# Kernel tuning notes

Hardware: AMD Instinct MI355X
Metric: run time of the kernel (lower is better)

## Reference

```python
import jax, jax.numpy as jnp
import numpy as np

DIM = 1024
HIDDEN = 2816
NUM_EXPERTS = 8
TOP_K = 2
BATCH, SEQ = 2, 2048


def setup_inputs() -> dict:
    key = jax.random.key(0)
    kx, k1, k2, k3, kg = jax.random.split(key, 5)
    x = jax.random.normal(kx, (BATCH, SEQ, DIM), dtype=jnp.float32)
    # merged expert weights, layout (num_experts * hidden, dim) as in torch module
    w1 = jax.random.normal(k1, (NUM_EXPERTS * HIDDEN, DIM), dtype=jnp.float32) * 0.02
    w2 = jax.random.normal(k2, (NUM_EXPERTS * HIDDEN, DIM), dtype=jnp.float32) * 0.02
    w3 = jax.random.normal(k3, (NUM_EXPERTS * HIDDEN, DIM), dtype=jnp.float32) * 0.02
    gate_w = jax.random.normal(kg, (NUM_EXPERTS, DIM), dtype=jnp.float32) * 0.02
    return {"x": x, "w1": w1, "w2": w2, "w3": w3, "gate_w": gate_w}


def reference(x, w1, w2, w3, gate_w):
    input_shape = x.shape
    xt = x.reshape(-1, input_shape[-1])  # (T, D)
    T = xt.shape[0]
    # gating: softmax in fp32, top-k, renormalize selected weights
    logits = xt @ gate_w.T  # (T, E)
    probs = jax.nn.softmax(logits.astype(jnp.float32), axis=-1)
    weights, selected = jax.lax.top_k(probs, TOP_K)  # (T, K)
    weights = weights / jnp.sum(weights, axis=-1, keepdims=True)
    weights = weights.astype(x.dtype)
    # combine weights per expert: (T, E)
    combine = jnp.sum(jax.nn.one_hot(selected, NUM_EXPERTS, dtype=x.dtype) * weights[..., None], axis=1)
    # per-expert SwiGLU FFN: h = silu(x W1_e^T) * (x W3_e^T); out_e = h @ W2_e
    W1 = w1.reshape(NUM_EXPERTS, HIDDEN, DIM)
    W2 = w2.reshape(NUM_EXPERTS, HIDDEN, DIM)
    W3 = w3.reshape(NUM_EXPERTS, HIDDEN, DIM)
    y = jnp.zeros((T, DIM), dtype=x.dtype)
    for e in range(NUM_EXPERTS):  # fixed small expert loop
        h = jax.nn.silu(xt @ W1[e].T) * (xt @ W3[e].T)  # (T, H)
        y = y + (h @ W2[e]) * combine[:, e:e + 1]
    return y.reshape(input_shape)
```

## Files before the change

kernel.cpp:

```cpp
#include <hip/hip_runtime.h>
#include <cstddef>
#include <cstdint>

#define T_TOK 4096
#define DIM   1024
#define HID   2816
#define NE    8
#define TOPK  2
#define CAP   9216
#define NRT   72
#define BM    128
#define BN    64
#define BK    32

#define WS_COUNTS  0
#define WS_CURSORS 64
#define WS_OFFSETS 128
#define WS_TILE_E  256
#define WS_SEL     1024
#define WS_WTS     33792
#define WS_ATOK    66560
#define WS_AW      103424
#define WS_XHI     140288
#define WS_XLO     8528896
#define WS_IMG     16917504

typedef __attribute__((ext_vector_type(8))) short bf16x8;
typedef __attribute__((ext_vector_type(8))) unsigned short u16x8;
typedef __attribute__((ext_vector_type(4))) float f32x4;

#define GL16(gp, lp) __builtin_amdgcn_global_load_lds( \
    (const __attribute__((address_space(1))) unsigned int*)(gp), \
    (__attribute__((address_space(3))) unsigned int*)(lp), 16, 0, 0)

__device__ __forceinline__ unsigned short f2bf(float f) {
  unsigned int u = __builtin_bit_cast(unsigned int, f);
  unsigned int r = u + 0x7FFFu + ((u >> 16) & 1u);
  return (unsigned short)(r >> 16);
}
__device__ __forceinline__ float bf2f(unsigned short s) {
  unsigned int u = ((unsigned int)s) << 16;
  return __builtin_bit_cast(float, u);
}
__device__ __forceinline__ void split2(float f, unsigned short& hi, unsigned short& lo) {
  hi = f2bf(f);
  lo = f2bf(f - bf2f(hi));
}

__global__ __launch_bounds__(256) void gate_kernel(
    const float* __restrict__ x, const float* __restrict__ gw,
    int* __restrict__ sel, float* __restrict__ wts, int* __restrict__ counts)
{
  const int wave = threadIdx.x >> 6;
  const int lane = threadIdx.x & 63;
  const int t = blockIdx.x * 4 + wave;
  const float* xr = x + (size_t)t * DIM;
  float acc[NE] = {0.f, 0.f, 0.f, 0.f, 0.f, 0.f, 0.f, 0.f};
#pragma unroll 4
  for (int j = 0; j < DIM / 64; ++j) {
    const int d = lane + 64 * j;
    const float xv = xr[d];
#pragma unroll
    for (int e = 0; e < NE; ++e) acc[e] = fmaf(xv, gw[e * DIM + d], acc[e]);
  }
#pragma unroll
  for (int m = 32; m > 0; m >>= 1) {
#pragma unroll
    for (int e = 0; e < NE; ++e) acc[e] += __shfl_xor(acc[e], m, 64);
  }
  if (lane == 0) {
    float mx = acc[0];
#pragma unroll
    for (int e = 1; e < NE; ++e) mx = fmaxf(mx, acc[e]);
    float ex[NE];
#pragma unroll
    for (int e = 0; e < NE; ++e) ex[e] = __expf(acc[e] - mx);
    int e0 = 0; float p0 = ex[0];
#pragma unroll
    for (int e = 1; e < NE; ++e) if (ex[e] > p0) { p0 = ex[e]; e0 = e; }
    int e1 = -1; float p1 = -1.f;
#pragma unroll
    for (int e = 0; e < NE; ++e) if (e != e0 && ex[e] > p1) { p1 = ex[e]; e1 = e; }
    const float inv = 1.f / (p0 + p1);
    sel[2 * t + 0] = e0; sel[2 * t + 1] = e1;
    wts[2 * t + 0] = p0 * inv; wts[2 * t + 1] = p1 * inv;
    atomicAdd(&counts[e0], 1);
    atomicAdd(&counts[e1], 1);
  }
}

__global__ void offsets_kernel(const int* __restrict__ counts,
                               int* __restrict__ offsets, int* __restrict__ cursors,
                               int* __restrict__ tile_e)
{
  if (threadIdx.x == 0 && blockIdx.x == 0) {
    int off = 0;
    for (int e = 0; e < NE; ++e) {
      offsets[e] = off;
      cursors[e] = off;
      off += (counts[e] + 127) & ~127;
    }
    offsets[NE] = off;
    for (int t = 0; t < NRT; ++t) {
      const int r = t * BM;
      int ee = 0;
      while (ee < NE - 1 && r >= offsets[ee + 1]) ++ee;
      tile_e[t] = ee;
    }
  }
}

__global__ __launch_bounds__(256) void scatter_kernel(
    const int* __restrict__ sel, const float* __restrict__ wts,
    int* __restrict__ cursors, int* __restrict__ atok, float* __restrict__ aw)
{
  const int t = blockIdx.x * 256 + threadIdx.x;
  if (t < T_TOK) {
#pragma unroll
    for (int k = 0; k < TOPK; ++k) {
      const int e = sel[2 * t + k];
      const int pos = atomicAdd(&cursors[e], 1);
      atok[pos] = t;
      aw[pos] = wts[2 * t + k];
    }
  }
}

__global__ __launch_bounds__(256) void convert_x_kernel(
    const float* __restrict__ x, unsigned short* __restrict__ xhi,
    unsigned short* __restrict__ xlo)
{
  const size_t t = (size_t)blockIdx.x * 256 + threadIdx.x;
  const float* s = x + t * 8;
  u16x8 hi, lo;
#pragma unroll
  for (int q = 0; q < 8; ++q) {
    unsigned short h, l;
    split2(s[q], h, l);
    hi[q] = h; lo[q] = l;
  }
  *(u16x8*)&xhi[t * 8] = hi;
  *(u16x8*)&xlo[t * 8] = lo;
}

__global__ __launch_bounds__(256) void convert_w13_kernel(
    const float* __restrict__ w, unsigned short* __restrict__ img,
    int hc0, int nct1)
{
  const int g = blockIdx.x * 256 + threadIdx.x;
  const int c = g & 255;
  const int t = g >> 8;
  const int n15 = c & 15, ks = (c >> 4) & 3, nb = c >> 6;
  const int kt = t & 31;
  const int ec = t >> 5;
  const int ct = ec % nct1, e = ec / nct1;
  const float* src = w + ((size_t)e * HID + hc0 + ct * 64 + nb * 16 + n15) * DIM + kt * 32 + ks * 8;
  u16x8 hi, lo;
#pragma unroll
  for (int q = 0; q < 8; ++q) {
    unsigned short h, l;
    split2(src[q], h, l);
    hi[q] = h; lo[q] = l;
  }
  *(u16x8*)&img[(size_t)t * 4096 + c * 8] = hi;
  *(u16x8*)&img[(size_t)t * 4096 + 2048 + c * 8] = lo;
}

__global__ __launch_bounds__(256) void convert_w2_kernel(
    const float* __restrict__ w2, unsigned short* __restrict__ img,
    int hc0, int nkt2)
{
  const int f = blockIdx.x * 256 + threadIdx.x;
  const int n15 = f & 15;
  int t = f >> 4;
  const int ks = t & 3; t >>= 2;
  const int nb = t & 3; t >>= 2;
  const int kt = t % nkt2; t /= nkt2;
  const int ct2 = t & 15;
  const int e = t >> 4;
  const float* src = w2 + ((size_t)e * HID + hc0 + kt * 32 + ks * 8) * DIM + ct2 * 64 + nb * 16 + n15;
  u16x8 hi, lo;
#pragma unroll
  for (int q = 0; q < 8; ++q) {
    unsigned short h, l;
    split2(src[(size_t)q * DIM], h, l);
    hi[q] = h; lo[q] = l;
  }
  const size_t tile = ((size_t)(e * 16 + ct2) * nkt2 + kt) * 4096;
  const int off = nb * 512 + ks * 128 + n15 * 8;
  *(u16x8*)&img[tile + off] = hi;
  *(u16x8*)&img[tile + 2048 + off] = lo;
}

__global__ __launch_bounds__(256) void gemm1_kernel(
    const unsigned short* __restrict__ xhi, const unsigned short* __restrict__ xlo,
    const unsigned short* __restrict__ w1img, const unsigned short* __restrict__ w3img,
    const int* __restrict__ atok, const int* __restrict__ tile_e,
    const int* __restrict__ offsets, unsigned short* __restrict__ himg, int nct1)
{
  __shared__ __align__(16) unsigned short sAh[4096], sAl[4096];
  __shared__ __align__(16) unsigned short sB1h[2048], sB1l[2048], sB3h[2048], sB3l[2048];
  __shared__ int sToks[BM];

  const int orig = blockIdx.x;
  const int wg = (orig & 7) * (gridDim.x >> 3) + (orig >> 3);
  const int ct = wg / NRT, rt = wg % NRT;
  if (rt * BM >= offsets[NE]) return;
  const int nkt2 = nct1 * 2;
  const int tid = threadIdx.x, lane = tid & 63;
  const int wv = tid >> 6, wr = wv >> 1, wc = wv & 1;
  const int e = tile_e[rt];

  if (tid < BM) {
    const int tk = atok[rt * BM + tid];
    sToks[tid] = tk < 0 ? 0 : tk;
  }
  __syncthreads();

  const int rb0 = wv * 2;
  size_t asrc[2];
#pragma unroll
  for (int i = 0; i < 2; ++i) {
    const int row = (rb0 + i) * 16 + (lane & 15);
    asrc[i] = (size_t)sToks[row] * DIM + ((lane >> 4) * 8);
  }
  const size_t btile0 = ((size_t)(e * nct1 + ct) * 32) * 4096;
  const size_t boff = btile0 + wv * 512 + (size_t)lane * 8;

  const f32x4 vz = {0.f, 0.f, 0.f, 0.f};
  f32x4 acc1[4][2], acc3[4][2];
#pragma unroll
  for (int i = 0; i < 4; ++i)
#pragma unroll
    for (int j = 0; j < 2; ++j) { acc1[i][j] = vz; acc3[i][j] = vz; }

  for (int kt = 0; kt < DIM / BK; ++kt) {
    __syncthreads();
#pragma unroll
    for (int i = 0; i < 2; ++i) {
      GL16(xhi + asrc[i] + kt * 32, &sAh[(rb0 + i) * 512]);
      GL16(xlo + asrc[i] + kt * 32, &sAl[(rb0 + i) * 512]);
    }
    const size_t bk = boff + (size_t)kt * 4096;
    GL16(w1img + bk,        &sB1h[wv * 512]);
    GL16(w1img + bk + 2048, &sB1l[wv * 512]);
    GL16(w3img + bk,        &sB3h[wv * 512]);
    GL16(w3img + bk + 2048, &sB3l[wv * 512]);
    __syncthreads();

    bf16x8 ah[4], al[4], g1h[2], g1l[2], g3h[2], g3l[2];
#pragma unroll
    for (int ar = 0; ar < 4; ++ar) {
      const int rb = wr * 4 + ar;
      ah[ar] = *(const bf16x8*)&sAh[rb * 512 + lane * 8];
      al[ar] = *(const bf16x8*)&sAl[rb * 512 + lane * 8];
    }
#pragma unroll
    for (int bc = 0; bc < 2; ++bc) {
      const int cb = wc * 2 + bc;
      g1h[bc] = *(const bf16x8*)&sB1h[cb * 512 + lane * 8];
      g1l[bc] = *(const bf16x8*)&sB1l[cb * 512 + lane * 8];
      g3h[bc] = *(const bf16x8*)&sB3h[cb * 512 + lane * 8];
      g3l[bc] = *(const bf16x8*)&sB3l[cb * 512 + lane * 8];
    }
#pragma unroll
    for (int ar = 0; ar < 4; ++ar)
#pragma unroll
      for (int bc = 0; bc < 2; ++bc) {
        acc1[ar][bc] = __builtin_amdgcn_mfma_f32_16x16x32_bf16(ah[ar], g1h[bc], acc1[ar][bc], 0, 0, 0);
        acc1[ar][bc] = __builtin_amdgcn_mfma_f32_16x16x32_bf16(ah[ar], g1l[bc], acc1[ar][bc], 0, 0, 0);
        acc1[ar][bc] = __builtin_amdgcn_mfma_f32_16x16x32_bf16(al[ar], g1h[bc], acc1[ar][bc], 0, 0, 0);
        acc3[ar][bc] = __builtin_amdgcn_mfma_f32_16x16x32_bf16(ah[ar], g3h[bc], acc3[ar][bc], 0, 0, 0);
        acc3[ar][bc] = __builtin_amdgcn_mfma_f32_16x16x32_bf16(ah[ar], g3l[bc], acc3[ar][bc], 0, 0, 0);
        acc3[ar][bc] = __builtin_amdgcn_mfma_f32_16x16x32_bf16(al[ar], g3h[bc], acc3[ar][bc], 0, 0, 0);
      }
  }

  const size_t hbase = ((size_t)rt * nkt2 + (ct * 2 + wc)) * 8192;
#pragma unroll
  for (int ar = 0; ar < 4; ++ar)
#pragma unroll
    for (int bc = 0; bc < 2; ++bc)
#pragma unroll
      for (int r = 0; r < 4; ++r) {
        const float g = acc1[ar][bc][r];
        const float u = acc3[ar][bc][r];
        const float s = g / (1.f + __expf(-g));
        unsigned short h_, l_;
        split2(s * u, h_, l_);
        const int idx = (wr * 4 + ar) * 512 + (bc * 2 + ((lane >> 3) & 1)) * 128
                      + ((lane >> 4) * 4 + r) * 8 + (lane & 7);
        himg[hbase + idx] = h_;
        himg[hbase + 4096 + idx] = l_;
      }
}

__global__ __launch_bounds__(256) void gemm2_kernel(
    const unsigned short* __restrict__ himg, const unsigned short* __restrict__ w2img,
    const int* __restrict__ atok, const float* __restrict__ aw,
    const int* __restrict__ tile_e, const int* __restrict__ offsets,
    float* __restrict__ y, int nkt2)
{
  __shared__ __align__(16) unsigned short sAh[4096], sAl[4096];
  __shared__ __align__(16) unsigned short sBh[2048], sBl[2048];

  const int orig = blockIdx.x;
  const int wg = (orig & 7) * (gridDim.x >> 3) + (orig >> 3);
  const int ct2 = wg / NRT, rt = wg % NRT;
  if (rt * BM >= offsets[NE]) return;
  const int tid = threadIdx.x, lane = tid & 63;
  const int wv = tid >> 6, wr = wv >> 1, wc = wv & 1;
  const int e = tile_e[rt];

  const int rb0 = wv * 2;
  const size_t atile0 = (size_t)rt * nkt2 * 8192;
  const size_t btile0 = ((size_t)(e * 16 + ct2) * nkt2) * 4096;
  const size_t lane8 = (size_t)lane * 8;

  const f32x4 vz = {0.f, 0.f, 0.f, 0.f};
  f32x4 acc[4][2];
#pragma unroll
  for (int i = 0; i < 4; ++i)
#pragma unroll
    for (int j = 0; j < 2; ++j) acc[i][j] = vz;

  for (int kt = 0; kt < nkt2; ++kt) {
    __syncthreads();
    const size_t ab = atile0 + (size_t)kt * 8192;
#pragma unroll
    for (int i = 0; i < 2; ++i) {
      GL16(himg + ab + (rb0 + i) * 512 + lane8,        &sAh[(rb0 + i) * 512]);
      GL16(himg + ab + 4096 + (rb0 + i) * 512 + lane8, &sAl[(rb0 + i) * 512]);
    }
    const size_t bb = btile0 + (size_t)kt * 4096 + wv * 512 + lane8;
    GL16(w2img + bb,        &sBh[wv * 512]);
    GL16(w2img + bb + 2048, &sBl[wv * 512]);
    __syncthreads();

    bf16x8 ah[4], al[4], bh_[2], bl_[2];
#pragma unroll
    for (int ar = 0; ar < 4; ++ar) {
      const int rb = wr * 4 + ar;
      ah[ar] = *(const bf16x8*)&sAh[rb * 512 + lane * 8];
      al[ar] = *(const bf16x8*)&sAl[rb * 512 + lane * 8];
    }
#pragma unroll
    for (int bc = 0; bc < 2; ++bc) {
      const int cb = wc * 2 + bc;
      bh_[bc] = *(const bf16x8*)&sBh[cb * 512 + lane * 8];
      bl_[bc] = *(const bf16x8*)&sBl[cb * 512 + lane * 8];
    }
#pragma unroll
    for (int ar = 0; ar < 4; ++ar)
#pragma unroll
      for (int bc = 0; bc < 2; ++bc) {
        acc[ar][bc] = __builtin_amdgcn_mfma_f32_16x16x32_bf16(ah[ar], bh_[bc], acc[ar][bc], 0, 0, 0);
        acc[ar][bc] = __builtin_amdgcn_mfma_f32_16x16x32_bf16(ah[ar], bl_[bc], acc[ar][bc], 0, 0, 0);
        acc[ar][bc] = __builtin_amdgcn_mfma_f32_16x16x32_bf16(al[ar], bh_[bc], acc[ar][bc], 0, 0, 0);
      }
  }

#pragma unroll
  for (int ar = 0; ar < 4; ++ar)
#pragma unroll
    for (int r = 0; r < 4; ++r) {
      const int grow = rt * BM + wr * 64 + ar * 16 + (lane >> 4) * 4 + r;
      const int tok = atok[grow];
      if (tok >= 0) {
        const float wgt = aw[grow];
#pragma unroll
        for (int bc = 0; bc < 2; ++bc) {
          const int col = ct2 * BN + wc * 32 + bc * 16 + (lane & 15);
          atomicAdd(y + (size_t)tok * DIM + col, acc[ar][bc][r] * wgt);
        }
      }
    }
}

extern "C" void kernel_launch(void* const* d_in, const int* in_sizes, int n_in,
                              void* d_out, int out_size, void* d_ws, size_t ws_size,
                              hipStream_t stream) {
  const float* x  = (const float*)d_in[0];
  const float* w1 = (const float*)d_in[1];
  const float* w2 = (const float*)d_in[2];
  const float* w3 = (const float*)d_in[3];
  const float* gw = (const float*)d_in[4];
  float* y = (float*)d_out;

  char* ws = (char*)d_ws;
  int*   counts  = (int*)(ws + WS_COUNTS);
  int*   cursors = (int*)(ws + WS_CURSORS);
  int*   offsets = (int*)(ws + WS_OFFSETS);
  int*   tile_e  = (int*)(ws + WS_TILE_E);
  int*   sel     = (int*)(ws + WS_SEL);
  float* wts     = (float*)(ws + WS_WTS);
  int*   atok    = (int*)(ws + WS_ATOK);
  float* aw      = (float*)(ws + WS_AW);
  unsigned short* xhi = (unsigned short*)(ws + WS_XHI);
  unsigned short* xlo = (unsigned short*)(ws + WS_XLO);

  static const int chs[6] = {2816, 1408, 704, 256, 128, 64};
  int CH = 64;
  for (int i = 0; i < 6; ++i) {
    const size_t need = (size_t)WS_IMG + (size_t)chs[i] * 135168ull;
    if (need <= ws_size) { CH = chs[i]; break; }
  }
  const int nct1 = CH / 64, nkt2 = CH / 32;
  const size_t wimg_b = (size_t)CH * 32768ull;
  unsigned short* w1img = (unsigned short*)(ws + WS_IMG);
  unsigned short* w3img = (unsigned short*)(ws + WS_IMG + wimg_b);
  unsigned short* w2img = (unsigned short*)(ws + WS_IMG + 2 * wimg_b);
  unsigned short* himg  = (unsigned short*)(ws + WS_IMG + 3 * wimg_b);

  hipMemsetAsync(counts, 0, 8 * sizeof(int), stream);
  hipMemsetAsync(atok, 0xFF, CAP * sizeof(int), stream);
  hipMemsetAsync(y, 0, (size_t)T_TOK * DIM * sizeof(float), stream);

  gate_kernel<<<T_TOK / 4, 256, 0, stream>>>(x, gw, sel, wts, counts);
  offsets_kernel<<<1, 64, 0, stream>>>(counts, offsets, cursors, tile_e);
  scatter_kernel<<<T_TOK / 256, 256, 0, stream>>>(sel, wts, cursors, atok, aw);
  convert_x_kernel<<<(T_TOK * DIM / 8) / 256, 256, 0, stream>>>(x, xhi, xlo);

  for (int hc0 = 0; hc0 < HID; hc0 += CH) {
    const int wblk = 8 * nct1 * 32;
    convert_w13_kernel<<<wblk, 256, 0, stream>>>(w1, w1img, hc0, nct1);
    convert_w13_kernel<<<wblk, 256, 0, stream>>>(w3, w3img, hc0, nct1);
    convert_w2_kernel<<<128 * nkt2, 256, 0, stream>>>(w2, w2img, hc0, nkt2);
    gemm1_kernel<<<NRT * nct1, 256, 0, stream>>>(xhi, xlo, w1img, w3img, atok, tile_e, offsets, himg, nct1);
    gemm2_kernel<<<NRT * 16, 256, 0, stream>>>(himg, w2img, atok, aw, tile_e, offsets, y, nkt2);
  }
}
```

Baseline: 1.111 ms.

## Store weight hi/lo splits in plain row-major layout with coalesced conversion

Weight conversion now writes separate hi and lo bf16 planes in simple row-major layout: W1/W3 are converted with fully contiguous reads and writes, and W2 is transposed through an LDS tile so both the reads and the writes are coalesced. Before this, the conversion kernels wrote tiled images, and the W2 path read with a DIM stride. The GEMM kernels now load B fragments from these row-major planes using strided row addresses instead of contiguous tile blocks. The aim is to make the fp32-to-bf16 conversion passes cheaper, at the risk of less contiguous B loads inside the GEMMs.

```diff
diff --git a/kernel.cpp b/kernel.cpp
--- a/kernel.cpp
+++ b/kernel.cpp
@@ -143,58 +143,67 @@
   *(u16x8*)&xlo[t * 8] = lo;
 }
 
-__global__ __launch_bounds__(256) void convert_w13_kernel(
-    const float* __restrict__ w, unsigned short* __restrict__ img,
-    int hc0, int nct1)
-{
-  const int g = blockIdx.x * 256 + threadIdx.x;
-  const int c = g & 255;
-  const int t = g >> 8;
-  const int n15 = c & 15, ks = (c >> 4) & 3, nb = c >> 6;
-  const int kt = t & 31;
-  const int ec = t >> 5;
-  const int ct = ec % nct1, e = ec / nct1;
-  const float* src = w + ((size_t)e * HID + hc0 + ct * 64 + nb * 16 + n15) * DIM + kt * 32 + ks * 8;
+__global__ __launch_bounds__(256) void convert_w13s_kernel(
+    const float* __restrict__ w, unsigned short* __restrict__ hi_img,
+    unsigned short* __restrict__ lo_img, int hc0, int CH)
+{
+  const int e = blockIdx.y;
+  const size_t off = ((size_t)blockIdx.x * 256 + threadIdx.x) * 8;
+  const float* s = w + ((size_t)e * HID + hc0) * DIM + off;
   u16x8 hi, lo;
 #pragma unroll
   for (int q = 0; q < 8; ++q) {
     unsigned short h, l;
-    split2(src[q], h, l);
+    split2(s[q], h, l);
     hi[q] = h; lo[q] = l;
   }
-  *(u16x8*)&img[(size_t)t * 4096 + c * 8] = hi;
-  *(u16x8*)&img[(size_t)t * 4096 + 2048 + c * 8] = lo;
-}
-
-__global__ __launch_bounds__(256) void convert_w2_kernel(
-    const float* __restrict__ w2, unsigned short* __restrict__ img,
-    int hc0, int nkt2)
-{
-  const int f = blockIdx.x * 256 + threadIdx.x;
-  const int n15 = f & 15;
-  int t = f >> 4;
-  const int ks = t & 3; t >>= 2;
-  const int nb = t & 3; t >>= 2;
-  const int kt = t % nkt2; t /= nkt2;
-  const int ct2 = t & 15;
-  const int e = t >> 4;
-  const float* src = w2 + ((size_t)e * HID + hc0 + kt * 32 + ks * 8) * DIM + ct2 * 64 + nb * 16 + n15;
-  u16x8 hi, lo;
-#pragma unroll
-  for (int q = 0; q < 8; ++q) {
-    unsigned short h, l;
-    split2(src[(size_t)q * DIM], h, l);
-    hi[q] = h; lo[q] = l;
-  }
-  const size_t tile = ((size_t)(e * 16 + ct2) * nkt2 + kt) * 4096;
-  const int off = nb * 512 + ks * 128 + n15 * 8;
-  *(u16x8*)&img[tile + off] = hi;
-  *(u16x8*)&img[tile + 2048 + off] = lo;
+  const size_t d = (size_t)e * CH * DIM + off;
+  *(u16x8*)&hi_img[d] = hi;
+  *(u16x8*)&lo_img[d] = lo;
+}
+
+__global__ __launch_bounds__(256) void convert_w2t_kernel(
+    const float* __restrict__ w2, unsigned short* __restrict__ hi_img,
+    unsigned short* __restrict__ lo_img, int hc0, int CH)
+{
+  __shared__ float tile[64][65];
+  const int kb = blockIdx.x;
+  const int nb = blockIdx.y;
+  const int e  = blockIdx.z;
+  const int tid = threadIdx.x;
+
+  const int r0 = tid >> 4;
+  const int c4 = (tid & 15) * 4;
+#pragma unroll
+  for (int i = 0; i < 4; ++i) {
+    const int k = r0 + i * 16;
+    const float4 v = *(const float4*)(w2 + ((size_t)e * HID + hc0 + kb * 64 + k) * DIM + nb * 64 + c4);
+    tile[k][c4 + 0] = v.x; tile[k][c4 + 1] = v.y;
+    tile[k][c4 + 2] = v.z; tile[k][c4 + 3] = v.w;
+  }
+  __syncthreads();
+
+#pragma unroll
+  for (int i = 0; i < 2; ++i) {
+    const int c = tid + 256 * i;
+    const int n = c >> 3, k8 = (c & 7) * 8;
+    u16x8 hi, lo;
+#pragma unroll
+    for (int q = 0; q < 8; ++q) {
+      unsigned short h, l;
+      split2(tile[k8 + q][n], h, l);
+      hi[q] = h; lo[q] = l;
+    }
+    const size_t d = ((size_t)e * DIM + nb * 64 + n) * CH + kb * 64 + k8;
+    *(u16x8*)&hi_img[d] = hi;
+    *(u16x8*)&lo_img[d] = lo;
+  }
 }
 
 __global__ __launch_bounds__(256) void gemm1_kernel(
     const unsigned short* __restrict__ xhi, const unsigned short* __restrict__ xlo,
-    const unsigned short* __restrict__ w1img, const unsigned short* __restrict__ w3img,
+    const unsigned short* __restrict__ w1hi, const unsigned short* __restrict__ w1lo,
+    const unsigned short* __restrict__ w3hi, const unsigned short* __restrict__ w3lo,
     const int* __restrict__ atok, const int* __restrict__ tile_e,
     const int* __restrict__ offsets, unsigned short* __restrict__ himg, int nct1)
 {
@@ -206,6 +215,7 @@
   const int wg = (orig & 7) * (gridDim.x >> 3) + (orig >> 3);
   const int ct = wg / NRT, rt = wg % NRT;
   if (rt * BM >= offsets[NE]) return;
+  const int CH = nct1 * 64;
   const int nkt2 = nct1 * 2;
   const int tid = threadIdx.x, lane = tid & 63;
   const int wv = tid >> 6, wr = wv >> 1, wc = wv & 1;
@@ -224,8 +234,7 @@
     const int row = (rb0 + i) * 16 + (lane & 15);
     asrc[i] = (size_t)sToks[row] * DIM + ((lane >> 4) * 8);
   }
-  const size_t btile0 = ((size_t)(e * nct1 + ct) * 32) * 4096;
-  const size_t boff = btile0 + wv * 512 + (size_t)lane * 8;
+  const size_t brow = ((size_t)e * CH + ct * 64 + wv * 16 + (lane & 15)) * DIM + ((lane >> 4) * 8);
 
   const f32x4 vz = {0.f, 0.f, 0.f, 0.f};
   f32x4 acc1[4][2], acc3[4][2];
@@ -241,11 +250,11 @@
       GL16(xhi + asrc[i] + kt * 32, &sAh[(rb0 + i) * 512]);
       GL16(xlo + asrc[i] + kt * 32, &sAl[(rb0 + i) * 512]);
     }
-    const size_t bk = boff + (size_t)kt * 4096;
-    GL16(w1img + bk,        &sB1h[wv * 512]);
-    GL16(w1img + bk + 2048, &sB1l[wv * 512]);
-    GL16(w3img + bk,        &sB3h[wv * 512]);
-    GL16(w3img + bk + 2048, &sB3l[wv * 512]);
+    const size_t bk = brow + (size_t)kt * 32;
+    GL16(w1hi + bk, &sB1h[wv * 512]);
+    GL16(w1lo + bk, &sB1l[wv * 512]);
+    GL16(w3hi + bk, &sB3h[wv * 512]);
+    GL16(w3lo + bk, &sB3l[wv * 512]);
     __syncthreads();
 
     bf16x8 ah[4], al[4], g1h[2], g1l[2], g3h[2], g3l[2];
@@ -296,7 +305,8 @@
 }
 
 __global__ __launch_bounds__(256) void gemm2_kernel(
-    const unsigned short* __restrict__ himg, const unsigned short* __restrict__ w2img,
+    const unsigned short* __restrict__ himg,
+    const unsigned short* __restrict__ w2thi, const unsigned short* __restrict__ w2tlo,
     const int* __restrict__ atok, const float* __restrict__ aw,
     const int* __restrict__ tile_e, const int* __restrict__ offsets,
     float* __restrict__ y, int nkt2)
@@ -308,13 +318,14 @@
   const int wg = (orig & 7) * (gridDim.x >> 3) + (orig >> 3);
   const int ct2 = wg / NRT, rt = wg % NRT;
   if (rt * BM >= offsets[NE]) return;
+  const int CH = nkt2 * 32;
   const int tid = threadIdx.x, lane = tid & 63;
   const int wv = tid >> 6, wr = wv >> 1, wc = wv & 1;
   const int e = tile_e[rt];
 
   const int rb0 = wv * 2;
   const size_t atile0 = (size_t)rt * nkt2 * 8192;
-  const size_t btile0 = ((size_t)(e * 16 + ct2) * nkt2) * 4096;
+  const size_t brow = ((size_t)e * DIM + ct2 * 64 + wv * 16 + (lane & 15)) * CH + ((lane >> 4) * 8);
   const size_t lane8 = (size_t)lane * 8;
 
   const f32x4 vz = {0.f, 0.f, 0.f, 0.f};
@@ -332,9 +343,9 @@
       GL16(himg + ab + (rb0 + i) * 512 + lane8,        &sAh[(rb0 + i) * 512]);
       GL16(himg + ab + 4096 + (rb0 + i) * 512 + lane8, &sAl[(rb0 + i) * 512]);
     }
-    const size_t bb = btile0 + (size_t)kt * 4096 + wv * 512 + lane8;
-    GL16(w2img + bb,        &sBh[wv * 512]);
-    GL16(w2img + bb + 2048, &sBl[wv * 512]);
+    const size_t bk = brow + (size_t)kt * 32;
+    GL16(w2thi + bk, &sBh[wv * 512]);
+    GL16(w2tlo + bk, &sBl[wv * 512]);
     __syncthreads();
 
     bf16x8 ah[4], al[4], bh_[2], bl_[2];
@@ -406,11 +417,14 @@
     if (need <= ws_size) { CH = chs[i]; break; }
   }
   const int nct1 = CH / 64, nkt2 = CH / 32;
-  const size_t wimg_b = (size_t)CH * 32768ull;
-  unsigned short* w1img = (unsigned short*)(ws + WS_IMG);
-  unsigned short* w3img = (unsigned short*)(ws + WS_IMG + wimg_b);
-  unsigned short* w2img = (unsigned short*)(ws + WS_IMG + 2 * wimg_b);
-  unsigned short* himg  = (unsigned short*)(ws + WS_IMG + 3 * wimg_b);
+  const size_t wimg_b = (size_t)CH * 16384ull;
+  unsigned short* w1hi  = (unsigned short*)(ws + WS_IMG);
+  unsigned short* w1lo  = (unsigned short*)(ws + WS_IMG + 1 * wimg_b);
+  unsigned short* w3hi  = (unsigned short*)(ws + WS_IMG + 2 * wimg_b);
+  unsigned short* w3lo  = (unsigned short*)(ws + WS_IMG + 3 * wimg_b);
+  unsigned short* w2thi = (unsigned short*)(ws + WS_IMG + 4 * wimg_b);
+  unsigned short* w2tlo = (unsigned short*)(ws + WS_IMG + 5 * wimg_b);
+  unsigned short* himg  = (unsigned short*)(ws + WS_IMG + 6 * wimg_b);
 
   hipMemsetAsync(counts, 0, 8 * sizeof(int), stream);
   hipMemsetAsync(atok, 0xFF, CAP * sizeof(int), stream);
@@ -422,11 +436,12 @@
   convert_x_kernel<<<(T_TOK * DIM / 8) / 256, 256, 0, stream>>>(x, xhi, xlo);
 
   for (int hc0 = 0; hc0 < HID; hc0 += CH) {
-    const int wblk = 8 * nct1 * 32;
-    convert_w13_kernel<<<wblk, 256, 0, stream>>>(w1, w1img, hc0, nct1);
-    convert_w13_kernel<<<wblk, 256, 0, stream>>>(w3, w3img, hc0, nct1);
-    convert_w2_kernel<<<128 * nkt2, 256, 0, stream>>>(w2, w2img, hc0, nkt2);
-    gemm1_kernel<<<NRT * nct1, 256, 0, stream>>>(xhi, xlo, w1img, w3img, atok, tile_e, offsets, himg, nct1);
-    gemm2_kernel<<<NRT * 16, 256, 0, stream>>>(himg, w2img, atok, aw, tile_e, offsets, y, nkt2);
-  }
-}
+    convert_w13s_kernel<<<dim3(CH / 2, 8), 256, 0, stream>>>(w1, w1hi, w1lo, hc0, CH);
+    convert_w13s_kernel<<<dim3(CH / 2, 8), 256, 0, stream>>>(w3, w3hi, w3lo, hc0, CH);
+    convert_w2t_kernel<<<dim3(CH / 64, 16, 8), 256, 0, stream>>>(w2, w2thi, w2tlo, hc0, CH);
+    gemm1_kernel<<<NRT * nct1, 256, 0, stream>>>(xhi, xlo, w1hi, w1lo, w3hi, w3lo,
+                                                 atok, tile_e, offsets, himg, nct1);
+    gemm2_kernel<<<NRT * 16, 256, 0, stream>>>(himg, w2thi, w2tlo,
+                                               atok, aw, tile_e, offsets, y, nkt2);
+  }
+}
```

Result: no change. 1.129 ms (+1.6%).
